# Kernel tuning notes

Hardware: AMD Instinct MI355X
Metric: run time of the kernel (lower is better)

Reference implementation:

```python
import jax, jax.numpy as jnp
import numpy as np

H, N, DIN, DOUT = 8, 2048, 768, 1024
HD = DOUT // H
SCALE = 1.0 / float(np.sqrt(HD))
NEG = -1e9
EPS = 1e-5


def setup_inputs() -> dict:
    key = jax.random.key(0)
    ks = jax.random.split(key, 20)
    w = lambda i, shape: jax.random.normal(ks[i], shape, jnp.float32) * 0.02
    inp = {
        'x': jax.random.normal(ks[0], (N, DIN), jnp.float32),
        'batch': jnp.sort(jax.random.randint(ks[1], (N,), 0, 64)).astype(jnp.int64)
                 if jax.config.jax_enable_x64 else jnp.sort(jax.random.randint(ks[1], (N,), 0, 64)),
        'motif_to_atom_attn': jax.random.normal(ks[2], (H, N, N), jnp.float32),
        'wq_w': w(3, (DIN, DOUT)), 'wq_b': jnp.zeros((DOUT,), jnp.float32),
        'wk_w': w(4, (DIN, DOUT)), 'wk_b': jnp.zeros((DOUT,), jnp.float32),
        'wv_w': w(5, (DIN, DOUT)), 'wv_b': jnp.zeros((DOUT,), jnp.float32),
        'wo_w': w(6, (DOUT, DIN)), 'wo_b': jnp.zeros((DIN,), jnp.float32),
        'ln_g': jnp.ones((DIN,), jnp.float32), 'ln_b': jnp.zeros((DIN,), jnp.float32),
        'alpha': jnp.float32(0.5), 'beta': jnp.float32(0.5),
        'gate_q_w': w(7, (DOUT, H)), 'gate_q_b': jnp.zeros((H,), jnp.float32),
        'gate_k_w': w(8, (DOUT, H)), 'gate_k_b': jnp.zeros((H,), jnp.float32),
        'head_interaction': jnp.eye(H, dtype=jnp.float32) + 0.01 * jax.random.normal(ks[9], (H, H), jnp.float32),
    }
    return inp


def reference(x, batch, motif_to_atom_attn, wq_w, wq_b, wk_w, wk_b, wv_w, wv_b,
              wo_w, wo_b, ln_g, ln_b, alpha, beta, gate_q_w, gate_q_b,
              gate_k_w, gate_k_b, head_interaction):
    n = x.shape[0]
    # projections -> [H, N, hd]
    q = (x @ wq_w + wq_b).reshape(n, H, HD).transpose(1, 0, 2)
    k = (x @ wk_w + wk_b).reshape(n, H, HD).transpose(1, 0, 2)
    v = (x @ wv_w + wv_b).reshape(n, H, HD).transpose(1, 0, 2)
    # scaled scores with block-diagonal batch mask [H, N, N]
    scores = jnp.einsum('hid,hjd->hij', q, k) * SCALE
    mask = batch[:, None] == batch[None, :]
    scores = jnp.where(mask[None, :, :], scores, NEG)
    attn_final = scores
    # Guide bias: torch permutes (N,N,H)->permute(2,1,0) which TRANSPOSES node dims
    attn_base = alpha * scores + beta * motif_to_atom_attn          # [H, N, N]
    attn_final = attn_final + jnp.swapaxes(attn_base, 1, 2)        # transposed in (i,j)
    # dynamic gating
    q_flat = q.transpose(1, 0, 2).reshape(n, DOUT)
    k_flat = k.transpose(1, 0, 2).reshape(n, DOUT)
    gq = jnp.tanh(q_flat @ gate_q_w + gate_q_b)                    # [N, H]
    gk = jnp.tanh(k_flat @ gate_k_w + gate_k_b)                    # [N, H]
    attn_final = attn_final + scores * (gq.T[:, :, None] + gk.T[:, None, :])
    # head interaction: res[m,i,j] = sum_h scores[h,i,j] * W[h,m]
    attn_final = attn_final + jnp.einsum('hij,hm->mij', scores, head_interaction)
    probs = jax.nn.softmax(attn_final, axis=-1)
    out = jnp.einsum('hij,hjd->hid', probs, v).transpose(1, 0, 2).reshape(n, DOUT)
    out = out @ wo_w + wo_b
    y = out + x
    mu = jnp.mean(y, axis=-1, keepdims=True)
    var = jnp.mean(jnp.square(y - mu), axis=-1, keepdims=True)
    y = (y - mu) * jax.lax.rsqrt(var + EPS) * ln_g + ln_b
    return y, attn_final
```

## Files before the change

### kernel.cpp

```cpp
#include <hip/hip_runtime.h>

#define NN    2048
#define DIN   768
#define DOUT  1024
#define NH    8
#define HD    128
#define SCALEF 0.08838834764831845f
#define NEGF  (-1.0e9f)
#define EPSF  1e-5f
#define EXPSHIFT 16.0f

typedef __attribute__((ext_vector_type(4))) float f32x4;
typedef __attribute__((ext_vector_type(8))) short bf16x8;

#define OFF_OBF  0
#define OFF_WOT  1048576
#define OFF_YACC 1441792
#define OFF_Q    3686400
#define OFF_K    4734976
#define OFF_VB   5783552
#define OFF_VT   6832128
#define OFF_XB   7880704
#define OFF_WT   8667136
#define OFF_GQ   9846784
#define OFF_GK   9863168

__device__ __forceinline__ short f2bf(float f) {
  union { float f; unsigned u; } v; v.f = f;
  unsigned r = v.u + 0x7FFF + ((v.u >> 16) & 1);
  return (short)(r >> 16);
}
__device__ __forceinline__ float bf2f(short s) {
  union { unsigned u; float f; } v; v.u = ((unsigned)(unsigned short)s) << 16;
  return v.f;
}

__global__ __launch_bounds__(256) void k_prep(const float* __restrict__ x,
                                              short* __restrict__ xb,
                                              const float* __restrict__ wq,
                                              const float* __restrict__ wk,
                                              const float* __restrict__ wv,
                                              short* __restrict__ Wt,
                                              const float* __restrict__ wo,
                                              short* __restrict__ wot) {
  const int bid = blockIdx.x;
  const int tid = threadIdx.x;
  if (bid < 1536) {
    int idx = bid * 256 + tid;
    float4 v = ((const float4*)x)[idx];
    union { short s[4]; float2 f; } u;
    u.s[0] = f2bf(v.x); u.s[1] = f2bf(v.y); u.s[2] = f2bf(v.z); u.s[3] = f2bf(v.w);
    ((float2*)xb)[idx] = u.f;
    return;
  }
  __shared__ float t[64][65];
  if (bid < 2112) {
    const int w = bid - 1536;
    const int z = w / 192, rem = w % 192;
    const int c0 = (rem % 16) * 64, k0 = (rem / 16) * 64;
    const float* Wm = (z == 0) ? wq : (z == 1) ? wk : wv;
#pragma unroll
    for (int l = 0; l < 4; ++l) {
      int f = tid + l * 256;
      int r = f >> 4, c4 = (f & 15) * 4;
      *(float4*)&t[r][c4] = *(const float4*)(Wm + (size_t)(k0 + r) * DOUT + c0 + c4);
    }
    __syncthreads();
    int r2 = tid >> 2, q = tid & 3;
    union { short s[16]; float4 f[2]; } buf;
#pragma unroll
    for (int jj = 0; jj < 16; ++jj) buf.s[jj] = f2bf(t[q * 16 + jj][r2]);
    short* dst = Wt + (size_t)z * (1024 * 768) + (size_t)(c0 + r2) * 768 + k0 + q * 16;
    ((float4*)dst)[0] = buf.f[0];
    ((float4*)dst)[1] = buf.f[1];
  } else {
    const int w = bid - 2112;
    const int c0 = (w % 12) * 64, k0 = (w / 12) * 64;
#pragma unroll
    for (int l = 0; l < 4; ++l) {
      int f = tid + l * 256;
      int r = f >> 4, c4 = (f & 15) * 4;
      *(float4*)&t[r][c4] = *(const float4*)(wo + (size_t)(k0 + r) * DIN + c0 + c4);
    }
    __syncthreads();
    int r2 = tid >> 2, q = tid & 3;
    union { short s[16]; float4 f[2]; } buf;
#pragma unroll
    for (int jj = 0; jj < 16; ++jj) buf.s[jj] = f2bf(t[q * 16 + jj][r2]);
    short* dst = wot + (size_t)(c0 + r2) * DOUT + k0 + q * 16;
    ((float4*)dst)[0] = buf.f[0];
    ((float4*)dst)[1] = buf.f[1];
  }
}

__global__ __launch_bounds__(256) void k_qkv(const short* __restrict__ xb,
                                             const short* __restrict__ Wt,
                                             const float* __restrict__ bq,
                                             const float* __restrict__ bk,
                                             const float* __restrict__ bv,
                                             short* __restrict__ Qb,
                                             short* __restrict__ Kb,
                                             short* __restrict__ Vb) {
  const int n0 = blockIdx.x * 128;
  const int i0 = blockIdx.y * 64;
  const int mat = n0 >> 10;
  const int cl = n0 & 1023;
  const float* bias = (mat == 0) ? bq : (mat == 1) ? bk : bv;
  const short* Wm = Wt + (size_t)mat * (1024 * 768);
  const int tid = threadIdx.x, lane = tid & 63, wave = tid >> 6;
  const int ln = lane & 15, quad = lane >> 4, q8 = quad * 8;
  __shared__ __align__(16) short Bs[2][128][56];
  const int brow = tid >> 1, bseg = (tid & 1) * 16;
  const short* gB = Wm + (size_t)(cl + brow) * DIN + bseg;
  {
    bf16x8 b0 = *(const bf16x8*)(gB);
    bf16x8 b1 = *(const bf16x8*)(gB + 8);
    *(bf16x8*)&Bs[0][brow][bseg] = b0;
    *(bf16x8*)&Bs[0][brow][bseg + 8] = b1;
  }
  bf16x8 cb0 = *(const bf16x8*)(gB + 32);
  bf16x8 cb1 = *(const bf16x8*)(gB + 40);
  __syncthreads();
  f32x4 acc[8];
#pragma unroll
  for (int nt = 0; nt < 8; ++nt) acc[nt] = (f32x4){0.f, 0.f, 0.f, 0.f};
  const short* a0 = xb + (size_t)(i0 + 16 * wave + ln) * DIN + q8;
  for (int ks = 0; ks < 24; ++ks) {
    const int bufc = ks & 1;
    bf16x8 nb0, nb1;
    if (ks < 22) {
      nb0 = *(const bf16x8*)(gB + 32 * (ks + 2));
      nb1 = *(const bf16x8*)(gB + 32 * (ks + 2) + 8);
    }
    bf16x8 A0 = *(const bf16x8*)(a0 + 32 * ks);
#pragma unroll
    for (int nt = 0; nt < 8; ++nt) {
      bf16x8 B = *(const bf16x8*)&Bs[bufc][16 * nt + ln][q8];
      acc[nt] = __builtin_amdgcn_mfma_f32_16x16x32_bf16(A0, B, acc[nt], 0, 0, 0);
    }
    if (ks < 23) {
      *(bf16x8*)&Bs[bufc ^ 1][brow][bseg] = cb0;
      *(bf16x8*)&Bs[bufc ^ 1][brow][bseg + 8] = cb1;
    }
    __syncthreads();
    if (ks < 22) { cb0 = nb0; cb1 = nb1; }
  }
#pragma unroll
  for (int nt = 0; nt < 8; ++nt) {
    int cg = cl + 16 * nt + ln;
    float bb = bias[cg];
#pragma unroll
    for (int reg = 0; reg < 4; ++reg) {
      int rr = i0 + 16 * wave + quad * 4 + reg;
      short s = f2bf(acc[nt][reg] + bb);
      if (mat == 2) {
        Vb[(size_t)rr * 1024 + cg] = s;
      } else {
        int h = cg >> 7, d = cg & 127;
        (mat == 0 ? Qb : Kb)[((size_t)h * NN + rr) * HD + d] = s;
      }
    }
  }
}

__global__ __launch_bounds__(256) void k_vtg(const short* __restrict__ Qb,
                                             const short* __restrict__ Kb,
                                             const float* __restrict__ gqw,
                                             const float* __restrict__ gqb,
                                             const float* __restrict__ gkw,
                                             const float* __restrict__ gkb,
                                             float* __restrict__ GQ,
                                             float* __restrict__ GK,
                                             const short* __restrict__ Vb,
                                             short* __restrict__ Vt) {
  const int bid = blockIdx.x;
  const int tid = threadIdx.x;
  __shared__ __align__(16) char smem[41216];
  if (bid < 128) {
    const int i0 = bid * 16;
    const int lane = tid & 63, wave = tid >> 6;
    const int ln = lane & 15, quad = lane >> 4, q8 = quad * 8;
    auto BqT = (short (*)[1032])(smem);
    auto BkT = (short (*)[1032])(smem + 16512);
    auto pQ  = (float (*)[16][16])(smem + 33024);
    auto pK  = (float (*)[16][16])(smem + 37120);
#pragma unroll
    for (int e = 0; e < 4; ++e) {
      const int k = tid * 4 + e;
      float4 a = *(const float4*)(gqw + (size_t)k * NH);
      float4 b = *(const float4*)(gqw + (size_t)k * NH + 4);
      BqT[0][k] = f2bf(a.x); BqT[1][k] = f2bf(a.y);
      BqT[2][k] = f2bf(a.z); BqT[3][k] = f2bf(a.w);
      BqT[4][k] = f2bf(b.x); BqT[5][k] = f2bf(b.y);
      BqT[6][k] = f2bf(b.z); BqT[7][k] = f2bf(b.w);
      float4 c = *(const float4*)(gkw + (size_t)k * NH);
      float4 d = *(const float4*)(gkw + (size_t)k * NH + 4);
      BkT[0][k] = f2bf(c.x); BkT[1][k] = f2bf(c.y);
      BkT[2][k] = f2bf(c.z); BkT[3][k] = f2bf(c.w);
      BkT[4][k] = f2bf(d.x); BkT[5][k] = f2bf(d.y);
      BkT[6][k] = f2bf(d.z); BkT[7][k] = f2bf(d.w);
    }
    __syncthreads();
    f32x4 aq = (f32x4){0.f, 0.f, 0.f, 0.f};
    f32x4 ak = (f32x4){0.f, 0.f, 0.f, 0.f};
    const int lnb = ln & 7;
#pragma unroll
    for (int c = 0; c < 8; ++c) {
      const int k0 = wave * 256 + c * 32;
      const int h = k0 >> 7, dd = (k0 & 127) + q8;
      bf16x8 Aq = *(const bf16x8*)(Qb + ((size_t)h * NN + i0 + ln) * HD + dd);
      bf16x8 Bq = *(const bf16x8*)&BqT[lnb][k0 + q8];
      aq = __builtin_amdgcn_mfma_f32_16x16x32_bf16(Aq, Bq, aq, 0, 0, 0);
      bf16x8 Ak = *(const bf16x8*)(Kb + ((size_t)h * NN + i0 + ln) * HD + dd);
      bf16x8 Bk = *(const bf16x8*)&BkT[lnb][k0 + q8];
      ak = __builtin_amdgcn_mfma_f32_16x16x32_bf16(Ak, Bk, ak, 0, 0, 0);
    }
#pragma unroll
    for (int reg = 0; reg < 4; ++reg) {
      pQ[wave][quad * 4 + reg][ln] = aq[reg];
      pK[wave][quad * 4 + reg][ln] = ak[reg];
    }
    __syncthreads();
    const int row = tid >> 4, col = tid & 15;
    if (col < NH) {
      float sq = pQ[0][row][col] + pQ[1][row][col] + pQ[2][row][col] + pQ[3][row][col];
      GQ[(size_t)(i0 + row) * NH + col] = tanhf(sq + gqb[col]);
      float sk = pK[0][row][col] + pK[1][row][col] + pK[2][row][col] + pK[3][row][col];
      GK[(size_t)(i0 + row) * NH + col] = tanhf(sk + gkb[col]);
    }
  } else {
    auto t = (short (*)[136])(smem);
    const int w = bid - 128;
    const int i0 = (w & 31) * 64, h = w >> 5;
#pragma unroll
    for (int l = 0; l < 2; ++l) {
      int f = tid + l * 256;
      int r = f >> 3, c8 = (f & 7) * 16;
      const short* src = Vb + (size_t)(i0 + r) * 1024 + h * HD + c8;
      *(bf16x8*)&t[r][c8] = *(const bf16x8*)src;
      *(bf16x8*)&t[r][c8 + 8] = *(const bf16x8*)(src + 8);
    }
    __syncthreads();
    int d = tid >> 1, half = tid & 1;
    union { short s[32]; float4 f[4]; } buf;
#pragma unroll
    for (int ii = 0; ii < 32; ++ii) buf.s[ii] = t[32 * half + ii][d];
    short* dst = Vt + (size_t)h * (HD * NN) + (size_t)d * NN + i0 + 32 * half;
#pragma unroll
    for (int q = 0; q < 4; ++q) ((float4*)dst)[q] = buf.f[q];
  }
}

__global__ __launch_bounds__(256, 4) void k_sa(const short* __restrict__ Qb,
                                               const short* __restrict__ Kb,
                                               const int* __restrict__ batch,
                                               const float* __restrict__ motif,
                                               const float* __restrict__ GQ,
                                               const float* __restrict__ GK,
                                               const float* __restrict__ Wh,
                                               const float* __restrict__ alpha_p,
                                               const float* __restrict__ beta_p,
                                               float* __restrict__ ATTN) {
  const unsigned gid = blockIdx.y * gridDim.x + blockIdx.x;
  const unsigned xcd = gid & 7, idx = gid >> 3;
  const unsigned P = xcd + 8 * (idx >> 8);
  const unsigned r256 = idx & 255;
  const unsigned bx = 16 * (P & 3) + (r256 & 15);
  const unsigned by = 16 * (P >> 2) + (r256 >> 4);
  const int i0 = by * 32, j0 = bx * 32;

  const int tid = threadIdx.x, lane = tid & 63, wave = tid >> 6;
  const int wr = wave >> 1, wc = wave & 1;
  const int ln = lane & 15, quad = lane >> 4, q8 = quad * 8;

  __shared__ __align__(16) char smem[38400];
  auto Qs  = (short (*)[32][136])(smem);
  auto Ks  = (short (*)[32][136])(smem + 17408);
  auto oL8 = (float (*)[34])(smem);
  auto gqL = (float (*)[12])(smem + 34816);
  auto gkL = (float (*)[12])(smem + 36352);
  float* sW = (float*)(smem + 37888);

  const int rA = 16 * wr + quad * 4;
  const int cA = 16 * wc + ln;

  const int srow = tid >> 3, sseg = (tid & 7) * 16;
  const short* gQ0 = Qb + (size_t)(i0 + srow) * HD + sseg;
  const short* gK0 = Kb + (size_t)(j0 + srow) * HD + sseg;
  const size_t hstep = (size_t)NN * HD;

  {
    bf16x8 q0 = *(const bf16x8*)(gQ0);
    bf16x8 q1 = *(const bf16x8*)(gQ0 + 8);
    bf16x8 k0 = *(const bf16x8*)(gK0);
    bf16x8 k1 = *(const bf16x8*)(gK0 + 8);
    *(bf16x8*)&Qs[0][srow][sseg] = q0;
    *(bf16x8*)&Qs[0][srow][sseg + 8] = q1;
    *(bf16x8*)&Ks[0][srow][sseg] = k0;
    *(bf16x8*)&Ks[0][srow][sseg + 8] = k1;
  }
  bf16x8 cq0 = *(const bf16x8*)(gQ0 + hstep);
  bf16x8 cq1 = *(const bf16x8*)(gQ0 + hstep + 8);
  bf16x8 ck0 = *(const bf16x8*)(gK0 + hstep);
  bf16x8 ck1 = *(const bf16x8*)(gK0 + hstep + 8);
  if (tid < 64) {
    const int half = tid >> 5, r = tid & 31;
    const float* src = (half ? GK : GQ) + (size_t)((half ? j0 : i0) + r) * NH;
    float4 a = *(const float4*)src;
    float4 b = *(const float4*)(src + 4);
    float* dst = half ? &gkL[r][0] : &gqL[r][0];
    *(float4*)dst = a;
    *(float4*)(dst + 4) = b;
    sW[tid] = Wh[tid];
  }
  const int4 bi4 = *(const int4*)(batch + i0 + rA);
  const int bj = batch[j0 + cA];
  const float alpha = alpha_p[0], beta = beta_p[0];
  __syncthreads();

  f32x4 accS[NH], accT[NH];
#pragma unroll
  for (int h = 0; h < NH; ++h) {
    accS[h] = (f32x4){0.f, 0.f, 0.f, 0.f};
    accT[h] = (f32x4){0.f, 0.f, 0.f, 0.f};
  }

#pragma unroll
  for (int h = 0; h < NH; ++h) {
    const int bufc = h & 1;
    bf16x8 nq0, nq1, nk0, nk1;
    if (h < 6) {
      const short* gq_ = gQ0 + (size_t)(h + 2) * hstep;
      const short* gk_ = gK0 + (size_t)(h + 2) * hstep;
      nq0 = *(const bf16x8*)(gq_);
      nq1 = *(const bf16x8*)(gq_ + 8);
      nk0 = *(const bf16x8*)(gk_);
      nk1 = *(const bf16x8*)(gk_ + 8);
    }
#pragma unroll
    for (int ks = 0; ks < 4; ++ks) {
      bf16x8 aS = *(const bf16x8*)&Qs[bufc][16 * wr + ln][ks * 32 + q8];
      bf16x8 bS = *(const bf16x8*)&Ks[bufc][16 * wc + ln][ks * 32 + q8];
      accS[h] = __builtin_amdgcn_mfma_f32_16x16x32_bf16(aS, bS, accS[h], 0, 0, 0);
      bf16x8 aT = *(const bf16x8*)&Ks[bufc][16 * wr + ln][ks * 32 + q8];
      bf16x8 bT = *(const bf16x8*)&Qs[bufc][16 * wc + ln][ks * 32 + q8];
      accT[h] = __builtin_amdgcn_mfma_f32_16x16x32_bf16(aT, bT, accT[h], 0, 0, 0);
    }
    if (h < 7) {
      *(bf16x8*)&Qs[bufc ^ 1][srow][sseg] = cq0;
      *(bf16x8*)&Qs[bufc ^ 1][srow][sseg + 8] = cq1;
      *(bf16x8*)&Ks[bufc ^ 1][srow][sseg] = ck0;
      *(bf16x8*)&Ks[bufc ^ 1][srow][sseg + 8] = ck1;
    }
    __syncthreads();
    if (h < 6) { cq0 = nq0; cq1 = nq1; ck0 = nk0; ck1 = nk1; }
  }

  int okm[4];
  okm[0] = (bi4.x == bj); okm[1] = (bi4.y == bj);
  okm[2] = (bi4.z == bj); okm[3] = (bi4.w == bj);
#pragma unroll
  for (int reg = 0; reg < 4; ++reg)
#pragma unroll
    for (int h = 0; h < NH; ++h)
      accS[h][reg] = okm[reg] ? accS[h][reg] * SCALEF : NEGF;

  union { float4 v; float f[4]; } moc, mon, mo2;
  moc.v = *(const float4*)(motif + ((size_t)(j0 + cA)) * NN + i0 + rA);
  mon.v = *(const float4*)(motif + ((size_t)(NN + j0 + cA)) * NN + i0 + rA);
#pragma unroll
  for (int h = 0; h < NH; ++h) {
    if (h < 6)
      mo2.v = *(const float4*)(motif + ((size_t)(h + 2) * NN + j0 + cA) * NN + i0 + rA);
    float w8[NH];
#pragma unroll
    for (int h2 = 0; h2 < NH; ++h2) w8[h2] = sW[h2 * NH + h];
    const float gkj = gkL[cA][h];
#pragma unroll
    for (int reg = 0; reg < 4; ++reg) {
      float tv = okm[reg] ? accT[h][reg] * SCALEF : NEGF;
      float hm = 0.f;
#pragma unroll
      for (int h2 = 0; h2 < NH; ++h2) hm = fmaf(accS[h2][reg], w8[h2], hm);
      float o = accS[h][reg] * (1.f + gqL[rA + reg][h] + gkj) +
                alpha * tv + beta * moc.f[reg] + hm;
      oL8[h * 32 + rA + reg][cA] = o;
    }
    moc.v = mon.v;
    mon.v = mo2.v;
  }
  __syncthreads();

  const int orow = tid >> 3, oslot = (tid & 7) * 4;
#pragma unroll
  for (int h = 0; h < NH; ++h) {
    float2 a = *(const float2*)&oL8[h * 32 + orow][oslot];
    float2 b = *(const float2*)&oL8[h * 32 + orow][oslot + 2];
    float4 ov = float4{a.x, a.y, b.x, b.y};
    *(float4*)(ATTN + ((size_t)h * NN + i0 + orow) * NN + j0 + oslot) = ov;
  }
}

__global__ __launch_bounds__(256, 4) void k_pv(const float* __restrict__ ATTN,
                                               const short* __restrict__ Vt,
                                               short* __restrict__ Obf) {
  const int bid = blockIdx.x;
  const int h = bid & 7;
  const int i0 = (bid >> 3) * 16;
  const int tid = threadIdx.x, lane = tid & 63, wave = tid >> 6;
  const int ln = lane & 15, quad = lane >> 4, q8 = quad * 8;
  __shared__ float accL[4][16][140];
  __shared__ float SUML[4][16];
  const int jbase = wave * 512;
  const float* arow = ATTN + ((size_t)h * NN + i0 + ln) * NN + jbase;
  const short* vbase = Vt + (size_t)h * (HD * NN) + jbase;
  f32x4 acc[8];
#pragma unroll
  for (int nt = 0; nt < 8; ++nt) acc[nt] = (f32x4){0.f, 0.f, 0.f, 0.f};
  float rowsum = 0.f;
  bf16x8 vc[8];
#pragma unroll
  for (int nt = 0; nt < 8; ++nt)
    vc[nt] = *(const bf16x8*)(vbase + (size_t)(16 * nt + ln) * NN + q8);
  float4 u1 = *(const float4*)(arow + q8);
  float4 u2 = *(const float4*)(arow + q8 + 4);
#pragma unroll
  for (int c = 0; c < 16; ++c) {
    const int jk = c * 32;
    bf16x8 vn[8];
    float4 n1, n2;
    if (c < 15) {
#pragma unroll
      for (int nt = 0; nt < 8; ++nt)
        vn[nt] = *(const bf16x8*)(vbase + (size_t)(16 * nt + ln) * NN + jk + 32 + q8);
      n1 = *(const float4*)(arow + jk + 32 + q8);
      n2 = *(const float4*)(arow + jk + 32 + q8 + 4);
    }
    float p0 = __expf(u1.x - EXPSHIFT), p1 = __expf(u1.y - EXPSHIFT);
    float p2 = __expf(u1.z - EXPSHIFT), p3 = __expf(u1.w - EXPSHIFT);
    float p4 = __expf(u2.x - EXPSHIFT), p5 = __expf(u2.y - EXPSHIFT);
    float p6 = __expf(u2.z - EXPSHIFT), p7 = __expf(u2.w - EXPSHIFT);
    rowsum += ((p0 + p1) + (p2 + p3)) + ((p4 + p5) + (p6 + p7));
    bf16x8 a;
    a[0] = f2bf(p0); a[1] = f2bf(p1); a[2] = f2bf(p2); a[3] = f2bf(p3);
    a[4] = f2bf(p4); a[5] = f2bf(p5); a[6] = f2bf(p6); a[7] = f2bf(p7);
#pragma unroll
    for (int nt = 0; nt < 8; ++nt)
      acc[nt] = __builtin_amdgcn_mfma_f32_16x16x32_bf16(a, vc[nt], acc[nt], 0, 0, 0);
    if (c < 15) {
#pragma unroll
      for (int nt = 0; nt < 8; ++nt) vc[nt] = vn[nt];
      u1 = n1; u2 = n2;
    }
  }
  rowsum += __shfl_xor(rowsum, 16);
  rowsum += __shfl_xor(rowsum, 32);
  if (lane < 16) SUML[wave][ln] = rowsum;
#pragma unroll
  for (int nt = 0; nt < 8; ++nt)
#pragma unroll
    for (int reg = 0; reg < 4; ++reg)
      accL[wave][quad * 4 + reg][16 * nt + ln] = acc[nt][reg];
  __syncthreads();
  const int r = tid >> 4, d0 = (tid & 15) * 8;
  const float inv = 1.0f / (SUML[0][r] + SUML[1][r] + SUML[2][r] + SUML[3][r]);
  union { short s[8]; bf16x8 v; } ob;
#pragma unroll
  for (int e = 0; e < 8; ++e) {
    float s = accL[0][r][d0 + e] + accL[1][r][d0 + e] +
              accL[2][r][d0 + e] + accL[3][r][d0 + e];
    ob.s[e] = f2bf(s * inv);
  }
  *(bf16x8*)(Obf + (size_t)(i0 + r) * DOUT + h * HD + d0) = ob.v;
}

__global__ __launch_bounds__(256) void k_outproj(const short* __restrict__ Obf,
                                                 const short* __restrict__ wot,
                                                 float* __restrict__ YACC) {
  const int n0 = blockIdx.x * 64;
  const int i0 = blockIdx.y * 32;
  const int tid = threadIdx.x, lane = tid & 63, wave = tid >> 6;
  const int ln = lane & 15, quad = lane >> 4, q8 = quad * 8;
  const int wr = wave & 1, wcol = wave >> 1;
  __shared__ __align__(16) short Bs[2][64][56];
  const int brow = tid >> 2, bseg = (tid & 3) * 8;
  const short* gB = wot + (size_t)(n0 + brow) * DOUT + bseg;
  {
    bf16x8 b0 = *(const bf16x8*)(gB);
    *(bf16x8*)&Bs[0][brow][bseg] = b0;
  }
  bf16x8 cb0 = *(const bf16x8*)(gB + 32);
  __syncthreads();
  f32x4 acc[2];
#pragma unroll
  for (int nt = 0; nt < 2; ++nt) acc[nt] = (f32x4){0.f, 0.f, 0.f, 0.f};
  const short* a0 = Obf + (size_t)(i0 + 16 * wr + ln) * DOUT + q8;
  for (int ks = 0; ks < 32; ++ks) {
    const int bufc = ks & 1;
    bf16x8 nb0;
    if (ks < 30) nb0 = *(const bf16x8*)(gB + 32 * (ks + 2));
    bf16x8 A0 = *(const bf16x8*)(a0 + 32 * ks);
#pragma unroll
    for (int nt = 0; nt < 2; ++nt) {
      bf16x8 B = *(const bf16x8*)&Bs[bufc][32 * wcol + 16 * nt + ln][q8];
      acc[nt] = __builtin_amdgcn_mfma_f32_16x16x32_bf16(A0, B, acc[nt], 0, 0, 0);
    }
    if (ks < 31) *(bf16x8*)&Bs[bufc ^ 1][brow][bseg] = cb0;
    __syncthreads();
    if (ks < 30) cb0 = nb0;
  }
#pragma unroll
  for (int nt = 0; nt < 2; ++nt) {
    int cg = n0 + 32 * wcol + 16 * nt + ln;
#pragma unroll
    for (int reg = 0; reg < 4; ++reg) {
      int rr = i0 + 16 * wr + quad * 4 + reg;
      YACC[(size_t)rr * DIN + cg] = acc[nt][reg];
    }
  }
}

__global__ __launch_bounds__(256) void k_ln(const float* __restrict__ YACC,
                                            const float* __restrict__ x,
                                            const float* __restrict__ wo_b,
                                            const float* __restrict__ g,
                                            const float* __restrict__ b,
                                            float* __restrict__ y) {
  const int i = blockIdx.x;
  const int tid = threadIdx.x;
  const int lane = tid & 63, wave = tid >> 6;
  float v[3];
#pragma unroll
  for (int t = 0; t < 3; ++t) {
    int cc = tid + t * 256;
    v[t] = YACC[(size_t)i * DIN + cc] + wo_b[cc] + x[(size_t)i * DIN + cc];
  }
  __shared__ float p1[4], p2[4];
  float s = v[0] + v[1] + v[2];
#pragma unroll
  for (int off = 1; off < 64; off <<= 1) s += __shfl_xor(s, off);
  if (lane == 0) p1[wave] = s;
  __syncthreads();
  const float mu = (p1[0] + p1[1] + p1[2] + p1[3]) * (1.0f / DIN);
  float q = 0.f;
#pragma unroll
  for (int t = 0; t < 3; ++t) {
    float d = v[t] - mu;
    q += d * d;
  }
#pragma unroll
  for (int off = 1; off < 64; off <<= 1) q += __shfl_xor(q, off);
  if (lane == 0) p2[wave] = q;
  __syncthreads();
  const float rs = rsqrtf((p2[0] + p2[1] + p2[2] + p2[3]) * (1.0f / DIN) + EPSF);
#pragma unroll
  for (int t = 0; t < 3; ++t) {
    int cc = tid + t * 256;
    y[(size_t)i * DIN + cc] = (v[t] - mu) * rs * g[cc] + b[cc];
  }
}

extern "C" void kernel_launch(void* const* d_in, const int* in_sizes, int n_in,
                              void* d_out, int out_size, void* d_ws, size_t ws_size,
                              hipStream_t stream) {
  (void)in_sizes; (void)n_in; (void)out_size; (void)ws_size;
  const float* x       = (const float*)d_in[0];
  const int*   batch   = (const int*)d_in[1];
  const float* motif   = (const float*)d_in[2];
  const float* wq_w    = (const float*)d_in[3];
  const float* wq_b    = (const float*)d_in[4];
  const float* wk_w    = (const float*)d_in[5];
  const float* wk_b    = (const float*)d_in[6];
  const float* wv_w    = (const float*)d_in[7];
  const float* wv_b    = (const float*)d_in[8];
  const float* wo_w    = (const float*)d_in[9];
  const float* wo_b    = (const float*)d_in[10];
  const float* ln_g    = (const float*)d_in[11];
  const float* ln_b    = (const float*)d_in[12];
  const float* alpha_p = (const float*)d_in[13];
  const float* beta_p  = (const float*)d_in[14];
  const float* gq_w    = (const float*)d_in[15];
  const float* gq_b    = (const float*)d_in[16];
  const float* gk_w    = (const float*)d_in[17];
  const float* gk_b    = (const float*)d_in[18];
  const float* headW   = (const float*)d_in[19];

  float* y    = (float*)d_out;
  float* ATTN = (float*)d_out + (size_t)NN * DIN;
  float* ws   = (float*)d_ws;
  short* Obf  = (short*)(ws + OFF_OBF);
  short* wot  = (short*)(ws + OFF_WOT);
  float* YACC = ws + OFF_YACC;
  short* Qb   = (short*)(ws + OFF_Q);
  short* Kb   = (short*)(ws + OFF_K);
  short* Vb   = (short*)(ws + OFF_VB);
  short* Vt   = (short*)(ws + OFF_VT);
  short* xb   = (short*)(ws + OFF_XB);
  short* Wt   = (short*)(ws + OFF_WT);
  float* GQ   = ws + OFF_GQ;
  float* GK   = ws + OFF_GK;

  k_prep<<<2304, 256, 0, stream>>>(x, xb, wq_w, wk_w, wv_w, Wt, wo_w, wot);
  k_qkv<<<dim3(24, 32), 256, 0, stream>>>(xb, Wt, wq_b, wk_b, wv_b, Qb, Kb, Vb);
  k_vtg<<<384, 256, 0, stream>>>(Qb, Kb, gq_w, gq_b, gk_w, gk_b, GQ, GK, Vb, Vt);
  k_sa<<<dim3(64, 64), 256, 0, stream>>>(Qb, Kb, batch, motif, GQ, GK, headW,
                                         alpha_p, beta_p, ATTN);
  k_pv<<<1024, 256, 0, stream>>>(ATTN, Vt, Obf);
  k_outproj<<<dim3(12, 64), 256, 0, stream>>>(Obf, wot, YACC);
  k_ln<<<NN, 256, 0, stream>>>(YACC, x, wo_b, ln_g, ln_b, y);
}
```

Baseline: 453.8 us.

## Shrink score kernel LDS by single-buffering Q/K and per-head output staging

The score kernel drops from double-buffered Q/K tiles to a single buffer, and writes the output tile one head at a time through a small staging array instead of an 8-head buffer. This cuts shared memory per block from about 38 KB to about 20 KB, so more blocks can be resident per CU. In exchange it adds extra __syncthreads per head, which serialises the Q/K refill against the MFMA work and the output store against the epilogue. It also adds a redundant no-op store to BkT in the gating kernel.

```diff
diff --git a/kernel.cpp b/kernel.cpp
--- a/kernel.cpp
+++ b/kernel.cpp
@@ -198,6 +198,7 @@
       BkT[0][k] = f2bf(c.x); BkT[1][k] = f2bf(c.y);
       BkT[2][k] = f2bf(c.z); BkT[3][k] = f2bf(c.w);
       BkT[4][k] = f2bf(d.x); BkT[5][k] = f2bf(d.y);
+      BkT[6][k] = f2bf(d.w == d.w ? d.w : d.w);
       BkT[6][k] = f2bf(d.z); BkT[7][k] = f2bf(d.w);
     }
     __syncthreads();
@@ -273,13 +274,13 @@
   const int wr = wave >> 1, wc = wave & 1;
   const int ln = lane & 15, quad = lane >> 4, q8 = quad * 8;
 
-  __shared__ __align__(16) char smem[38400];
-  auto Qs  = (short (*)[32][136])(smem);
-  auto Ks  = (short (*)[32][136])(smem + 17408);
-  auto oL8 = (float (*)[34])(smem);
-  auto gqL = (float (*)[12])(smem + 34816);
-  auto gkL = (float (*)[12])(smem + 36352);
-  float* sW = (float*)(smem + 37888);
+  __shared__ __align__(16) char smem[20736];
+  auto Qs  = (short (*)[136])(smem);
+  auto Ks  = (short (*)[136])(smem + 8704);
+  auto oL  = (float (*)[36])(smem);
+  auto gqL = (float (*)[12])(smem + 17408);
+  auto gkL = (float (*)[12])(smem + 18944);
+  float* sW = (float*)(smem + 20480);
 
   const int rA = 16 * wr + quad * 4;
   const int cA = 16 * wc + ln;
@@ -294,10 +295,10 @@
     bf16x8 q1 = *(const bf16x8*)(gQ0 + 8);
     bf16x8 k0 = *(const bf16x8*)(gK0);
     bf16x8 k1 = *(const bf16x8*)(gK0 + 8);
-    *(bf16x8*)&Qs[0][srow][sseg] = q0;
-    *(bf16x8*)&Qs[0][srow][sseg + 8] = q1;
-    *(bf16x8*)&Ks[0][srow][sseg] = k0;
-    *(bf16x8*)&Ks[0][srow][sseg + 8] = k1;
+    *(bf16x8*)&Qs[srow][sseg] = q0;
+    *(bf16x8*)&Qs[srow][sseg + 8] = q1;
+    *(bf16x8*)&Ks[srow][sseg] = k0;
+    *(bf16x8*)&Ks[srow][sseg + 8] = k1;
   }
   bf16x8 cq0 = *(const bf16x8*)(gQ0 + hstep);
   bf16x8 cq1 = *(const bf16x8*)(gQ0 + hstep + 8);
@@ -327,7 +328,6 @@
 
 #pragma unroll
   for (int h = 0; h < NH; ++h) {
-    const int bufc = h & 1;
     bf16x8 nq0, nq1, nk0, nk1;
     if (h < 6) {
       const short* gq_ = gQ0 + (size_t)(h + 2) * hstep;
@@ -339,20 +339,21 @@
     }
 #pragma unroll
     for (int ks = 0; ks < 4; ++ks) {
-      bf16x8 aS = *(const bf16x8*)&Qs[bufc][16 * wr + ln][ks * 32 + q8];
-      bf16x8 bS = *(const bf16x8*)&Ks[bufc][16 * wc + ln][ks * 32 + q8];
+      bf16x8 aS = *(const bf16x8*)&Qs[16 * wr + ln][ks * 32 + q8];
+      bf16x8 bS = *(const bf16x8*)&Ks[16 * wc + ln][ks * 32 + q8];
       accS[h] = __builtin_amdgcn_mfma_f32_16x16x32_bf16(aS, bS, accS[h], 0, 0, 0);
-      bf16x8 aT = *(const bf16x8*)&Ks[bufc][16 * wr + ln][ks * 32 + q8];
-      bf16x8 bT = *(const bf16x8*)&Qs[bufc][16 * wc + ln][ks * 32 + q8];
+      bf16x8 aT = *(const bf16x8*)&Ks[16 * wr + ln][ks * 32 + q8];
+      bf16x8 bT = *(const bf16x8*)&Qs[16 * wc + ln][ks * 32 + q8];
       accT[h] = __builtin_amdgcn_mfma_f32_16x16x32_bf16(aT, bT, accT[h], 0, 0, 0);
     }
+    __syncthreads();
     if (h < 7) {
-      *(bf16x8*)&Qs[bufc ^ 1][srow][sseg] = cq0;
-      *(bf16x8*)&Qs[bufc ^ 1][srow][sseg + 8] = cq1;
-      *(bf16x8*)&Ks[bufc ^ 1][srow][sseg] = ck0;
-      *(bf16x8*)&Ks[bufc ^ 1][srow][sseg + 8] = ck1;
-    }
-    __syncthreads();
+      *(bf16x8*)&Qs[srow][sseg] = cq0;
+      *(bf16x8*)&Qs[srow][sseg + 8] = cq1;
+      *(bf16x8*)&Ks[srow][sseg] = ck0;
+      *(bf16x8*)&Ks[srow][sseg + 8] = ck1;
+      __syncthreads();
+    }
     if (h < 6) { cq0 = nq0; cq1 = nq1; ck0 = nk0; ck1 = nk1; }
   }
 
@@ -365,6 +366,7 @@
     for (int h = 0; h < NH; ++h)
       accS[h][reg] = okm[reg] ? accS[h][reg] * SCALEF : NEGF;
 
+  const int orow = tid >> 3, oslot = (tid & 7) * 4;
   union { float4 v; float f[4]; } moc, mon, mo2;
   moc.v = *(const float4*)(motif + ((size_t)(j0 + cA)) * NN + i0 + rA);
   mon.v = *(const float4*)(motif + ((size_t)(NN + j0 + cA)) * NN + i0 + rA);
@@ -384,20 +386,14 @@
       for (int h2 = 0; h2 < NH; ++h2) hm = fmaf(accS[h2][reg], w8[h2], hm);
       float o = accS[h][reg] * (1.f + gqL[rA + reg][h] + gkj) +
                 alpha * tv + beta * moc.f[reg] + hm;
-      oL8[h * 32 + rA + reg][cA] = o;
-    }
+      oL[rA + reg][cA] = o;
+    }
+    __syncthreads();
+    float4 ov = *(const float4*)&oL[orow][oslot];
+    *(float4*)(ATTN + ((size_t)h * NN + i0 + orow) * NN + j0 + oslot) = ov;
+    if (h < 7) __syncthreads();
     moc.v = mon.v;
     mon.v = mo2.v;
-  }
-  __syncthreads();
-
-  const int orow = tid >> 3, oslot = (tid & 7) * 4;
-#pragma unroll
-  for (int h = 0; h < NH; ++h) {
-    float2 a = *(const float2*)&oL8[h * 32 + orow][oslot];
-    float2 b = *(const float2*)&oL8[h * 32 + orow][oslot + 2];
-    float4 ov = float4{a.x, a.y, b.x, b.y};
-    *(float4*)(ATTN + ((size_t)h * NN + i0 + orow) * NN + j0 + oslot) = ov;
   }
 }
 
```

After: 462.1 us. Within noise of the previous version (+1.8%).
